# Optimization experiments

Measured on AMD Instinct MI355X. Metric: run time of the kernel, lower is better.

Reference implementation:

```python
import jax, jax.numpy as jnp
import numpy as np

NY, NU, NHIDDEN = 64, 32, 512
T, BATCH = 512, 256
DAMP = 0.99


def setup_inputs() -> dict:
    key = jax.random.key(0)
    ks = jax.random.split(key, 8)
    nh2 = NHIDDEN // 2
    theta = jax.random.uniform(ks[0], (nh2,)) * (jnp.pi / 2)
    lmbd_real = DAMP * jnp.cos(theta)
    lmbd_imag = DAMP * jnp.sin(theta)
    B = jax.random.normal(ks[1], (NHIDDEN, NU)) / np.sqrt(NU) * np.sqrt(1.0 - DAMP ** 2)
    W_y2x = jax.random.normal(ks[2], (NHIDDEN, NY)) / np.sqrt(NY)
    b_y2x = jnp.zeros((NHIDDEN,), jnp.float32)
    W_x2y = jax.random.normal(ks[3], (NY, NHIDDEN)) / np.sqrt(NHIDDEN)
    b_x2y = jnp.zeros((NY,), jnp.float32)
    y0 = jax.random.normal(ks[4], (BATCH, NY), jnp.float32)
    U = jax.random.normal(ks[5], (T, BATCH, NU), jnp.float32)
    return {"y0": y0, "U": U, "lmbd_real": lmbd_real, "lmbd_imag": lmbd_imag,
            "B": B, "W_y2x": W_y2x, "b_y2x": b_y2x, "W_x2y": W_x2y, "b_x2y": b_x2y}


def reference(y0, U, lmbd_real, lmbd_imag, B, W_y2x, b_y2x, W_x2y, b_x2y):
    # x_{k+1} = x_k @ A^T + B u_k, where A = [[diag(lr), -diag(li)], [diag(li), diag(lr)]]
    # i.e. an elementwise complex rotation of the paired state halves.
    nh2 = lmbd_real.shape[0]
    Bu = jnp.einsum('tbu,hu->tbh', U, B)          # [T, batch, Nhidden]
    x0 = y0 @ W_y2x.T + b_y2x                     # [batch, Nhidden]

    def step(x, bu):
        xr, xi = x[..., :nh2], x[..., nh2:]
        nr = lmbd_real * xr - lmbd_imag * xi
        ni = lmbd_imag * xr + lmbd_real * xi
        xn = jnp.concatenate([nr, ni], axis=-1) + bu
        return xn, xn

    _, Xs = jax.lax.scan(step, x0, Bu)            # [T, batch, Nhidden]
    X = jnp.concatenate([x0[None], Xs], axis=0)   # [T+1, batch, Nhidden]
    Y = X @ W_x2y.T + b_x2y                       # [T+1, batch, Ny]
    return Y
```

## Files before the change

### kernel.cpp

```cpp
#include <hip/hip_runtime.h>


constexpr int NY  = 64;
constexpr int NU  = 32;
constexpr int NH  = 512;
constexpr int NH2 = 256;
constexpr int TT  = 512;
constexpr int BB  = 256;
constexpr int KK  = 16;
constexpr int NSS = TT / KK;

constexpr int USP = 40;
constexpr int XSP = 544;
constexpr int BUP = 516;
constexpr int PSP = 20;

typedef __attribute__((ext_vector_type(4))) short sh4;
typedef __attribute__((ext_vector_type(8))) short sh8;
typedef __attribute__((ext_vector_type(4))) float f32x4;

#define MFMA16(a, b, c) __builtin_amdgcn_mfma_f32_16x16x32_bf16((a), (b), (c), 0, 0, 0)

__device__ __forceinline__ unsigned short bfh(float x) {
    return (unsigned short)(__float_as_uint(x) >> 16);
}
__device__ __forceinline__ float bf2f(unsigned short h) {
    return __uint_as_float(((unsigned)h) << 16);
}
__device__ __forceinline__ void cvt4(const float4 f, sh4& vh, sh4& vl) {
    const float e[4] = { f.x, f.y, f.z, f.w };
#pragma unroll
    for (int j = 0; j < 4; ++j) {
        const unsigned short h = bfh(e[j]);
        vh[j] = (short)h;
        vl[j] = (short)bfh(e[j] - bf2f(h));
    }
}

__global__ __launch_bounds__(512, 2)
void lru_fused_kernel(const float* __restrict__ y0,
                      const float* __restrict__ U,
                      const float* __restrict__ lmr,
                      const float* __restrict__ lmi,
                      const float* __restrict__ Bmat,
                      const float* __restrict__ Wy2x,
                      const float* __restrict__ by2x,
                      const float* __restrict__ Wx2y,
                      const float* __restrict__ bx2y,
                      float* __restrict__ Y)
{
    const int b    = blockIdx.x;
    const int tid  = threadIdx.x;
    const int w    = tid >> 6;
    const int l    = tid & 63;
    const int lr16 = l & 15;
    const int lg   = l >> 4;

    __shared__ unsigned short us_h[2][64][USP], us_l[2][64][USP];
    __shared__ unsigned short xs_h[2][KK][XSP], xs_l[2][KK][XSP];
    __shared__ float          bu[KK][BUP];
    __shared__ float          psy[4][2][16][PSP];
    __shared__ float          y0s[NY];

    sh8 frg[32];
    float lamr = 0.f, lami = 0.f, xr = 0.f, xi = 0.f;
    float biasE = 0.f;
    int   xwrd  = 0;

    if (tid < NH2) {
#pragma unroll
        for (int q = 0; q < 8; ++q) {
            sh8 vh, vl;
#pragma unroll
            for (int h2 = 0; h2 < 2; ++h2) {
                const int hrow = (w << 7) + (q << 4) + lr16;
                const int u0   = (h2 << 4) + (lg << 2);
                const float4 f4 = *reinterpret_cast<const float4*>(&Bmat[hrow * NU + u0]);
                sh4 th, tl;
                cvt4(f4, th, tl);
#pragma unroll
                for (int j = 0; j < 4; ++j) { vh[h2 * 4 + j] = th[j]; vl[h2 * 4 + j] = tl[j]; }
            }
            frg[q] = vh;
            frg[8 + q] = vl;
        }
        lamr = lmr[tid];
        lami = lmi[tid];
        const int q_ = tid & 15, blk = tid >> 4;
        xwrd = blk * 16 + ((q_ & 7) >> 1) * 4 + (q_ >> 3) * 2 + (q_ & 1);
    } else {
        const int j = w - 4, ntp = j >> 1, kh = j & 1;
#pragma unroll
        for (int ntt = 0; ntt < 2; ++ntt) {
            const int n = ((ntp << 1) + ntt) * 16 + lr16;
            const float* Wn = Wx2y + n * NH;
#pragma unroll
            for (int ks = 0; ks < 8; ++ks) {
                sh8 vh, vl;
#pragma unroll
                for (int h2 = 0; h2 < 2; ++h2) {
                    const int k0 = (kh << 8) + (ks << 5) + (h2 << 4) + (lg << 2);
                    const int p0 = k0 >> 1;
                    const float e[4] = { Wn[p0], Wn[p0 + 256], Wn[p0 + 1], Wn[p0 + 257] };
#pragma unroll
                    for (int j2 = 0; j2 < 4; ++j2) {
                        const unsigned short h = bfh(e[j2]);
                        vh[h2 * 4 + j2] = (short)h;
                        vl[h2 * 4 + j2] = (short)bfh(e[j2] - bf2f(h));
                    }
                }
                frg[ntt * 8 + ks] = vh;
                frg[16 + ntt * 8 + ks] = vl;
            }
        }
        biasE = bx2y[(j << 4) + lr16];
    }

    const float4* Ug = reinterpret_cast<const float4*>(U);
    {
        const int i = tid, t = i >> 3, g = i & 7;
        const float4 f = Ug[((t * BB + b) << 3) + g];
        const int pos = (g < 4) ? (g << 3) : (((g - 4) << 3) + 4);
        sh4 vh, vl;
        cvt4(f, vh, vl);
        *reinterpret_cast<sh4*>(&us_h[0][t][pos]) = vh;
        *reinterpret_cast<sh4*>(&us_l[0][t][pos]) = vl;
    }
    if (tid < NY) y0s[tid] = y0[b * NY + tid];
    __syncthreads();

    if (tid < NH2) {
        const float* wr = &Wy2x[tid * NY];
        const float* wi = &Wy2x[(NH2 + tid) * NY];
        float a0 = 0, a1 = 0, a2 = 0, a3 = 0;
        float c0 = 0, c1 = 0, c2 = 0, c3 = 0;
#pragma unroll
        for (int y = 0; y < NY; y += 4) {
            a0 += wr[y + 0] * y0s[y + 0];
            a1 += wr[y + 1] * y0s[y + 1];
            a2 += wr[y + 2] * y0s[y + 2];
            a3 += wr[y + 3] * y0s[y + 3];
            c0 += wi[y + 0] * y0s[y + 0];
            c1 += wi[y + 1] * y0s[y + 1];
            c2 += wi[y + 2] * y0s[y + 2];
            c3 += wi[y + 3] * y0s[y + 3];
        }
        xr = by2x[tid]       + (a0 + a1) + (a2 + a3);
        xi = by2x[NH2 + tid] + (c0 + c1) + (c2 + c3);
        const unsigned short hr = bfh(xr), hi2 = bfh(xi);
        reinterpret_cast<unsigned*>(&xs_h[1][0][0])[xwrd] =
            (unsigned)hr | ((unsigned)hi2 << 16);
        reinterpret_cast<unsigned*>(&xs_l[1][0][0])[xwrd] =
            (unsigned)bfh(xr - bf2f(hr)) | ((unsigned)bfh(xi - bf2f(hi2)) << 16);
    }
    __syncthreads();

    float4 pf0, pf1;

    for (int st = 0; st <= NSS; ++st) {
        if (tid < NH2) {
            if (st < NSS) {
                const int su = (st >> 2) & 1, t0 = (st & 3) << 4;
                const sh8 auh = *reinterpret_cast<const sh8*>(&us_h[su][t0 + lr16][lg << 3]);
                const sh8 aul = *reinterpret_cast<const sh8*>(&us_l[su][t0 + lr16][lg << 3]);
#pragma unroll
                for (int q = 0; q < 8; ++q) {
                    f32x4 acc = (f32x4){0.f, 0.f, 0.f, 0.f};
                    acc = MFMA16(auh, frg[q], acc);
                    acc = MFMA16(aul, frg[q], acc);
                    acc = MFMA16(auh, frg[8 + q], acc);
                    const int h = (w << 7) + (q << 4) + lr16;
#pragma unroll
                    for (int r = 0; r < 4; ++r)
                        bu[(lg << 2) + r][h] = acc[r];
                }
            }
        } else {
            const int c = st >> 2;
            if ((st & 3) == 0 && c < 7 && st < NSS) {
                const int i0 = tid - NH2, i1 = tid;
                pf0 = Ug[(((((c + 1) << 6) + (i0 >> 3)) * BB + b) << 3) + (i0 & 7)];
                pf1 = Ug[(((((c + 1) << 6) + (i1 >> 3)) * BB + b) << 3) + (i1 & 7)];
            }
            const int sx = (st + 1) & 1;
            const int j = w - 4, kh = j & 1;
            f32x4 a0 = (f32x4){0.f, 0.f, 0.f, 0.f};
            f32x4 a1 = (f32x4){0.f, 0.f, 0.f, 0.f};
#pragma unroll
            for (int ks = 0; ks < 8; ++ks) {
                const int sp = (kh << 8) + (ks << 5) + (lg << 3);
                const sh8 axh = *reinterpret_cast<const sh8*>(&xs_h[sx][lr16][sp]);
                const sh8 axl = *reinterpret_cast<const sh8*>(&xs_l[sx][lr16][sp]);
                a0 = MFMA16(axh, frg[ks], a0);
                a0 = MFMA16(axl, frg[ks], a0);
                a0 = MFMA16(axh, frg[16 + ks], a0);
                a1 = MFMA16(axh, frg[8 + ks], a1);
                a1 = MFMA16(axl, frg[8 + ks], a1);
                a1 = MFMA16(axh, frg[24 + ks], a1);
            }
#pragma unroll
            for (int r = 0; r < 4; ++r) {
                psy[j][0][(lg << 2) + r][lr16] = a0[r];
                psy[j][1][(lg << 2) + r][lr16] = a1[r];
            }
        }
        __syncthreads();

        if (tid < NH2) {
            if (st < NSS) {
                const int sw = st & 1;
                unsigned* xh = reinterpret_cast<unsigned*>(&xs_h[sw][0][0]);
                unsigned* xl = reinterpret_cast<unsigned*>(&xs_l[sw][0][0]);
#pragma unroll
                for (int k = 0; k < KK; ++k) {
                    const float bur = bu[k][tid];
                    const float bui = bu[k][NH2 + tid];
                    const float nr = lamr * xr - lami * xi + bur;
                    const float ni = lami * xr + lamr * xi + bui;
                    xr = nr;
                    xi = ni;
                    const unsigned short hr = bfh(xr), hi2 = bfh(xi);
                    xh[k * (XSP / 2) + xwrd] = (unsigned)hr | ((unsigned)hi2 << 16);
                    xl[k * (XSP / 2) + xwrd] =
                        (unsigned)bfh(xr - bf2f(hr)) | ((unsigned)bfh(xi - bf2f(hi2)) << 16);
                }
            }
        } else {
            if ((st & 3) == 1 && (st >> 2) < 7) {
                const int ns = ((st >> 2) + 1) & 1;
#pragma unroll
                for (int v = 0; v < 2; ++v) {
                    const float4 f = v ? pf1 : pf0;
                    const int i = v ? tid : (tid - NH2);
                    const int t = i >> 3, g = i & 7;
                    const int pos = (g < 4) ? (g << 3) : (((g - 4) << 3) + 4);
                    sh4 vh, vl;
                    cvt4(f, vh, vl);
                    *reinterpret_cast<sh4*>(&us_h[ns][t][pos]) = vh;
                    *reinterpret_cast<sh4*>(&us_l[ns][t][pos]) = vl;
                }
            }
            const int j = w - 4;
            const int j0 = j & ~1;
#pragma unroll
            for (int r = 0; r < 4; ++r) {
                const int m = (lg << 2) + r;
                const float v = psy[j0][j & 1][m][lr16] + psy[j0 + 1][j & 1][m][lr16] + biasE;
                if (st == 0) {
                    if (m == 0) Y[b * NY + (j << 4) + lr16] = v;
                } else {
                    const int s = ((st - 1) << 4) + m + 1;
                    Y[(s * BB + b) * NY + (j << 4) + lr16] = v;
                }
            }
        }
        __syncthreads();
    }
}

extern "C" void kernel_launch(void* const* d_in, const int* in_sizes, int n_in,
                              void* d_out, int out_size, void* d_ws, size_t ws_size,
                              hipStream_t stream) {
    const float* y0   = (const float*)d_in[0];
    const float* U    = (const float*)d_in[1];
    const float* lmr  = (const float*)d_in[2];
    const float* lmi  = (const float*)d_in[3];
    const float* Bm   = (const float*)d_in[4];
    const float* Wy2x = (const float*)d_in[5];
    const float* by2x = (const float*)d_in[6];
    const float* Wx2y = (const float*)d_in[7];
    const float* bx2y = (const float*)d_in[8];
    float* Y = (float*)d_out;

    lru_fused_kernel<<<dim3(BB), dim3(512), 0, stream>>>(
        y0, U, lmr, lmi, Bm, Wy2x, by2x, Wx2y, bx2y, Y);
}
```

Before: 163.8 us.

## Interleave Bu layout, prefetch recurrence inputs, use packed bf16 convert and split MFMA chains

```diff
diff --git a/kernel.cpp b/kernel.cpp
--- a/kernel.cpp
+++ b/kernel.cpp
@@ -21,13 +21,13 @@
 
 #define MFMA16(a, b, c) __builtin_amdgcn_mfma_f32_16x16x32_bf16((a), (b), (c), 0, 0, 0)
 
-__device__ __forceinline__ unsigned short bfh(float x) {
+static __device__ __forceinline__ unsigned short bfh(float x) {
     return (unsigned short)(__float_as_uint(x) >> 16);
 }
-__device__ __forceinline__ float bf2f(unsigned short h) {
+static __device__ __forceinline__ float bf2f(unsigned short h) {
     return __uint_as_float(((unsigned)h) << 16);
 }
-__device__ __forceinline__ void cvt4(const float4 f, sh4& vh, sh4& vl) {
+static __device__ __forceinline__ void cvt4(const float4 f, sh4& vh, sh4& vl) {
     const float e[4] = { f.x, f.y, f.z, f.w };
 #pragma unroll
     for (int j = 0; j < 4; ++j) {
@@ -35,6 +35,25 @@
         vh[j] = (short)h;
         vl[j] = (short)bfh(e[j] - bf2f(h));
     }
+}
+static __device__ __forceinline__ unsigned cvtpk(float a, float b) {
+    unsigned r;
+    asm("v_cvt_pk_bf16_f32 %0, %1, %2" : "=v"(r) : "v"(a), "v"(b));
+    return r;
+}
+static __device__ __forceinline__ void xs_store(unsigned* xh, unsigned* xl, int idx,
+                                                float xr, float xi) {
+    const unsigned hp = cvtpk(xr, xi);
+    const float rr = __uint_as_float(hp << 16);
+    const float ri = __uint_as_float(hp & 0xffff0000u);
+    xh[idx] = hp;
+    xl[idx] = cvtpk(xr - rr, xi - ri);
+}
+static __device__ __forceinline__ void bar_lds() {
+    __builtin_amdgcn_sched_barrier(0);
+    asm volatile("s_waitcnt lgkmcnt(0)" ::: "memory");
+    __builtin_amdgcn_s_barrier();
+    __builtin_amdgcn_sched_barrier(0);
 }
 
 __global__ __launch_bounds__(512, 2)
@@ -147,11 +166,8 @@
         }
         xr = by2x[tid]       + (a0 + a1) + (a2 + a3);
         xi = by2x[NH2 + tid] + (c0 + c1) + (c2 + c3);
-        const unsigned short hr = bfh(xr), hi2 = bfh(xi);
-        reinterpret_cast<unsigned*>(&xs_h[1][0][0])[xwrd] =
-            (unsigned)hr | ((unsigned)hi2 << 16);
-        reinterpret_cast<unsigned*>(&xs_l[1][0][0])[xwrd] =
-            (unsigned)bfh(xr - bf2f(hr)) | ((unsigned)bfh(xi - bf2f(hi2)) << 16);
+        xs_store(reinterpret_cast<unsigned*>(&xs_h[1][0][0]),
+                 reinterpret_cast<unsigned*>(&xs_l[1][0][0]), xwrd, xr, xi);
     }
     __syncthreads();
 
@@ -170,59 +186,75 @@
                     acc = MFMA16(aul, frg[q], acc);
                     acc = MFMA16(auh, frg[8 + q], acc);
                     const int h = (w << 7) + (q << 4) + lr16;
+                    const int c = (h < NH2) ? (h << 1) : (((h - NH2) << 1) | 1);
 #pragma unroll
                     for (int r = 0; r < 4; ++r)
-                        bu[(lg << 2) + r][h] = acc[r];
+                        bu[(lg << 2) + r][c] = acc[r];
                 }
             }
         } else {
-            const int c = st >> 2;
-            if ((st & 3) == 0 && c < 7 && st < NSS) {
+            const int cc = st >> 2;
+            if ((st & 3) == 0 && cc < 7 && st < NSS) {
                 const int i0 = tid - NH2, i1 = tid;
-                pf0 = Ug[(((((c + 1) << 6) + (i0 >> 3)) * BB + b) << 3) + (i0 & 7)];
-                pf1 = Ug[(((((c + 1) << 6) + (i1 >> 3)) * BB + b) << 3) + (i1 & 7)];
+                pf0 = Ug[(((((cc + 1) << 6) + (i0 >> 3)) * BB + b) << 3) + (i0 & 7)];
+                pf1 = Ug[(((((cc + 1) << 6) + (i1 >> 3)) * BB + b) << 3) + (i1 & 7)];
             }
             const int sx = (st + 1) & 1;
             const int j = w - 4, kh = j & 1;
-            f32x4 a0 = (f32x4){0.f, 0.f, 0.f, 0.f};
-            f32x4 a1 = (f32x4){0.f, 0.f, 0.f, 0.f};
-#pragma unroll
-            for (int ks = 0; ks < 8; ++ks) {
+            f32x4 a0a = (f32x4){0.f, 0.f, 0.f, 0.f};
+            f32x4 a1a = (f32x4){0.f, 0.f, 0.f, 0.f};
+            f32x4 a0b = (f32x4){0.f, 0.f, 0.f, 0.f};
+            f32x4 a1b = (f32x4){0.f, 0.f, 0.f, 0.f};
+#pragma unroll
+            for (int ks = 0; ks < 4; ++ks) {
                 const int sp = (kh << 8) + (ks << 5) + (lg << 3);
                 const sh8 axh = *reinterpret_cast<const sh8*>(&xs_h[sx][lr16][sp]);
                 const sh8 axl = *reinterpret_cast<const sh8*>(&xs_l[sx][lr16][sp]);
-                a0 = MFMA16(axh, frg[ks], a0);
-                a0 = MFMA16(axl, frg[ks], a0);
-                a0 = MFMA16(axh, frg[16 + ks], a0);
-                a1 = MFMA16(axh, frg[8 + ks], a1);
-                a1 = MFMA16(axl, frg[8 + ks], a1);
-                a1 = MFMA16(axh, frg[24 + ks], a1);
-            }
+                a0a = MFMA16(axh, frg[ks], a0a);
+                a0a = MFMA16(axl, frg[ks], a0a);
+                a0a = MFMA16(axh, frg[16 + ks], a0a);
+                a1a = MFMA16(axh, frg[8 + ks], a1a);
+                a1a = MFMA16(axl, frg[8 + ks], a1a);
+                a1a = MFMA16(axh, frg[24 + ks], a1a);
+            }
+#pragma unroll
+            for (int ks = 4; ks < 8; ++ks) {
+                const int sp = (kh << 8) + (ks << 5) + (lg << 3);
+                const sh8 axh = *reinterpret_cast<const sh8*>(&xs_h[sx][lr16][sp]);
+                const sh8 axl = *reinterpret_cast<const sh8*>(&xs_l[sx][lr16][sp]);
+                a0b = MFMA16(axh, frg[ks], a0b);
+                a0b = MFMA16(axl, frg[ks], a0b);
+                a0b = MFMA16(axh, frg[16 + ks], a0b);
+                a1b = MFMA16(axh, frg[8 + ks], a1b);
+                a1b = MFMA16(axl, frg[8 + ks], a1b);
+                a1b = MFMA16(axh, frg[24 + ks], a1b);
+            }
+            const f32x4 A0 = a0a + a0b;
+            const f32x4 A1 = a1a + a1b;
 #pragma unroll
             for (int r = 0; r < 4; ++r) {
-                psy[j][0][(lg << 2) + r][lr16] = a0[r];
-                psy[j][1][(lg << 2) + r][lr16] = a1[r];
-            }
-        }
-        __syncthreads();
+                psy[j][0][(lg << 2) + r][lr16] = A0[r];
+                psy[j][1][(lg << 2) + r][lr16] = A1[r];
+            }
+        }
+        bar_lds();
 
         if (tid < NH2) {
             if (st < NSS) {
                 const int sw = st & 1;
                 unsigned* xh = reinterpret_cast<unsigned*>(&xs_h[sw][0][0]);
                 unsigned* xl = reinterpret_cast<unsigned*>(&xs_l[sw][0][0]);
+                float2 bu2[KK];
+#pragma unroll
+                for (int k = 0; k < KK; ++k)
+                    bu2[k] = *reinterpret_cast<const float2*>(&bu[k][tid << 1]);
 #pragma unroll
                 for (int k = 0; k < KK; ++k) {
-                    const float bur = bu[k][tid];
-                    const float bui = bu[k][NH2 + tid];
-                    const float nr = lamr * xr - lami * xi + bur;
-                    const float ni = lami * xr + lamr * xi + bui;
+                    const float nr = lamr * xr - lami * xi + bu2[k].x;
+                    const float ni = lami * xr + lamr * xi + bu2[k].y;
                     xr = nr;
                     xi = ni;
-                    const unsigned short hr = bfh(xr), hi2 = bfh(xi);
-                    xh[k * (XSP / 2) + xwrd] = (unsigned)hr | ((unsigned)hi2 << 16);
-                    xl[k * (XSP / 2) + xwrd] =
-                        (unsigned)bfh(xr - bf2f(hr)) | ((unsigned)bfh(xi - bf2f(hi2)) << 16);
+                    xs_store(xh, xl, k * (XSP / 2) + xwrd, xr, xi);
                 }
             }
         } else {
@@ -254,7 +286,7 @@
                 }
             }
         }
-        __syncthreads();
+        bar_lds();
     }
 }
 
```

Result: no change. 165.0 us (+0.7%).
